# Kernel optimization log

Measured on AMD Instinct MI355X. Metric: run time of the kernel, lower is better.

## Reference

```python
import jax, jax.numpy as jnp
import numpy as np


def setup_inputs() -> dict:
    key = jax.random.key(0)
    k1, k2, k3 = jax.random.split(key, 3)
    B, S, dk = 8, 4096, 64  # per-head tensors; dk = embedding_size / h = 1024 / 16
    q = jax.random.normal(k1, (B, S, dk), dtype=jnp.float32)
    k = jax.random.normal(k2, (B, S, dk), dtype=jnp.float32)
    v = jax.random.normal(k3, (B, S, dk), dtype=jnp.float32)
    return {"q": q, "k": k, "v": v}


def reference(q, k, v):
    dk = q.shape[-1]
    # QK = q @ k^T scaled by 1/dk (NOT 1/sqrt(dk) -- faithful to source)
    scores = jnp.einsum("bqd,bkd->bqk", q, k) / dk  # [B, S, S]
    # padding mask derived from exact-zero score entries: -inf where QK == 0
    pad_mask = jnp.where(scores == 0, -jnp.inf, 0.0)
    # look-ahead (causal) mask: 0 where i >= j else -inf
    S = scores.shape[-1]
    causal = jnp.where(
        jnp.arange(S)[:, None] >= jnp.arange(S)[None, :], 0.0, -jnp.inf
    )  # [S, S]
    scores = scores + pad_mask + causal
    attn = jax.nn.softmax(scores, axis=-1)
    # NaN cleanup for fully-masked rows (softmax over all -inf)
    attn = jnp.where(jnp.isnan(attn), 0.0, attn)
    return jnp.einsum("bqk,bkd->bqd", attn, v)
```

## Files before the change

### kernel.cpp

```cpp
#include <hip/hip_runtime.h>
#include <hip/hip_bf16.h>
#include <stdint.h>

#define S_LEN 4096
#define DK    64
#define BQ    64
#define BK    64

typedef __bf16 bf16x8  __attribute__((ext_vector_type(8)));
typedef float  f32x16  __attribute__((ext_vector_type(16)));

__device__ __forceinline__ short f2bf(float f) {
    union { __bf16 h; short s; } u; u.h = (__bf16)f; return u.s;
}
__device__ __forceinline__ short4 cvt4(float4 f) {
    short4 s; s.x = f2bf(f.x); s.y = f2bf(f.y); s.z = f2bf(f.z); s.w = f2bf(f.w); return s;
}

__device__ __forceinline__ uint32_t cvtpk_bf16(float lo, float hi) {
    uint32_t d;
    asm("v_cvt_pk_bf16_f32 %0, %1, %2" : "=&v"(d) : "v"(lo), "v"(hi));
    return d;
}
__device__ __forceinline__ void plswap(uint32_t& a, uint32_t& b) {
    asm("v_permlane32_swap_b32 %0, %1" : "+v"(a), "+v"(b));
}

__device__ __forceinline__ void gload_lds16(const void* g, void* l) {
    auto gp = reinterpret_cast<const uint32_t __attribute__((address_space(1)))*>(
        reinterpret_cast<uintptr_t>(g));
    auto lp = reinterpret_cast<uint32_t __attribute__((address_space(3)))*>(
        reinterpret_cast<uintptr_t>(l));
    __builtin_amdgcn_global_load_lds(gp, lp, 16, 0, 0);
}

__device__ __forceinline__ int swz(int row) {
    return ((row ^ (row >> 3)) & 7) << 3;
}

__global__ __launch_bounds__(256) void prep_kernel(
    const float* __restrict__ K, const float* __restrict__ V,
    short* __restrict__ WK, short* __restrict__ WV)
{
    const int t = blockIdx.x, b = blockIdx.y;
    const int tid = threadIdx.x;
    const size_t ibase = ((size_t)b * S_LEN + (size_t)t * 64) * DK;
    const size_t obase = ((size_t)b * 64 + t) * 4096;
    const int r0 = tid >> 4;
    const int c0 = (tid & 15) * 4;

    #pragma unroll
    for (int i = 0; i < 4; ++i) {
        const int row = r0 + 16 * i;
        const float4 f = *reinterpret_cast<const float4*>(K + ibase + (size_t)row * DK + c0);
        *reinterpret_cast<short4*>(WK + obase + row * 64 + (c0 ^ swz(row))) = cvt4(f);
    }
    float4 vf[4];
    #pragma unroll
    for (int j = 0; j < 4; ++j)
        vf[j] = *reinterpret_cast<const float4*>(V + ibase + (size_t)(4 * r0 + j) * DK + c0);
    #pragma unroll
    for (int jj = 0; jj < 4; ++jj) {
        const int d = c0 + jj;
        short4 sp;
        sp.x = f2bf(reinterpret_cast<const float*>(&vf[0])[jj]);
        sp.y = f2bf(reinterpret_cast<const float*>(&vf[1])[jj]);
        sp.z = f2bf(reinterpret_cast<const float*>(&vf[2])[jj]);
        sp.w = f2bf(reinterpret_cast<const float*>(&vf[3])[jj]);
        *reinterpret_cast<short4*>(WV + obase + d * 64 + ((4 * r0) ^ swz(d))) = sp;
    }
}

__global__ __launch_bounds__(512, 2) void attn_kernel(
    const float* __restrict__ Q, float* __restrict__ O,
    const short* __restrict__ WK, const short* __restrict__ WV)
{
    __shared__ __align__(16) short Ks[2][16384];
    __shared__ __align__(16) short Vts[2][16384];
    __shared__ float2 Ml[4][2][32];

    const int tid  = threadIdx.x;
    const int wave = tid >> 6;
    const int lane = tid & 63;
    const int q32  = lane & 31;
    const int hi   = lane >> 5;
    const int hi4  = hi * 4;
    const int hi8  = hi * 8;
    const int grp  = wave & 3;
    const int qsub = wave >> 2;

    const int batch = blockIdx.y;
    const size_t bo = (size_t)batch * S_LEN * DK;
    const short* WKb = WK + (size_t)batch * 262144;
    const short* WVb = WV + (size_t)batch * 262144;

    auto stage_quad = [&](int quad, int buf) {
        const char* gk = (const char*)(WKb + (size_t)quad * 16384) + wave * 1024 + lane * 16;
        const char* gv = (const char*)(WVb + (size_t)quad * 16384) + wave * 1024 + lane * 16;
        char* lk = (char*)(&Ks[buf][0]) + wave * 1024;
        char* lv = (char*)(&Vts[buf][0]) + wave * 1024;
        #pragma unroll
        for (int i = 0; i < 4; ++i) {
            gload_lds16(gk + i * 8192, lk + i * 8192);
            gload_lds16(gv + i * 8192, lv + i * 8192);
        }
    };

    const float NEG_INF = -__builtin_inff();
    const float QSCALE  = 0.015625f * 1.44269504088896341f;
    const float THR     = 8.0f;
    const int swz0 = swz(q32);
    const int swz1 = swz(32 + q32);

    #pragma unroll 1
    for (int qi = 0; qi < 2; ++qi) {
        const int qb = qi ? (int)blockIdx.x : 63 - (int)blockIdx.x;
        const int q0 = qb * BQ;
        const int ntiles = qb + 1;
        const int nquads = (ntiles + 3) >> 2;
        const int qrow   = q0 + 32 * qsub + q32;

        bf16x8 qf[4];
        {
            const float* Qr = Q + bo + (size_t)qrow * DK;
            #pragma unroll
            for (int s = 0; s < 4; ++s) {
                const float4 a = *reinterpret_cast<const float4*>(Qr + 16 * s + hi8);
                const float4 b = *reinterpret_cast<const float4*>(Qr + 16 * s + hi8 + 4);
                qf[s][0] = (__bf16)(a.x * QSCALE); qf[s][1] = (__bf16)(a.y * QSCALE);
                qf[s][2] = (__bf16)(a.z * QSCALE); qf[s][3] = (__bf16)(a.w * QSCALE);
                qf[s][4] = (__bf16)(b.x * QSCALE); qf[s][5] = (__bf16)(b.y * QSCALE);
                qf[s][6] = (__bf16)(b.z * QSCALE); qf[s][7] = (__bf16)(b.w * QSCALE);
            }
        }

        float m_run = NEG_INF, l_run = 0.f;
        f32x16 oa0, oa1;
        #pragma unroll
        for (int r = 0; r < 16; ++r) { oa0[r] = 0.f; oa1[r] = 0.f; }

        stage_quad(0, 0);
        __syncthreads();

        for (int p = 0; p < nquads; ++p) {
            const int kt = 4 * p + grp;
            const bool pf = (p + 1 < nquads);
            if (pf) stage_quad(p + 1, (p + 1) & 1);

            const short* Kt = &Ks[p & 1][grp * 4096];
            const short* Vt = &Vts[p & 1][grp * 4096];
            const bool act = (kt < ntiles);

            if (act) {
                f32x16 sa0, sa1;
                #pragma unroll
                for (int r = 0; r < 16; ++r) { sa0[r] = 0.f; sa1[r] = 0.f; }
                __builtin_amdgcn_s_setprio(1);
                #pragma unroll
                for (int s = 0; s < 4; ++s) {
                    const int col = 16 * s + hi8;
                    const bf16x8 kf0 = *reinterpret_cast<const bf16x8*>(&Kt[q32 * 64 + (col ^ swz0)]);
                    const bf16x8 kf1 = *reinterpret_cast<const bf16x8*>(&Kt[(32 + q32) * 64 + (col ^ swz1)]);
                    sa0 = __builtin_amdgcn_mfma_f32_32x32x16_bf16(kf0, qf[s], sa0, 0, 0, 0);
                    sa1 = __builtin_amdgcn_mfma_f32_32x32x16_bf16(kf1, qf[s], sa1, 0, 0, 0);
                }
                __builtin_amdgcn_s_setprio(0);

                float ma[4] = {NEG_INF, NEG_INF, NEG_INF, NEG_INF};
                if (kt == qb) {
                    const int keybase = kt * BK + hi4;
                    #pragma unroll
                    for (int r = 0; r < 16; ++r) {
                        const int kl = (r & 3) + 8 * (r >> 2);
                        if (keybase + kl > qrow) sa0[r] = NEG_INF;
                        ma[r & 3] = fmaxf(ma[r & 3], sa0[r]);
                        if (keybase + kl + 32 > qrow) sa1[r] = NEG_INF;
                        ma[r & 3] = fmaxf(ma[r & 3], sa1[r]);
                    }
                } else {
                    #pragma unroll
                    for (int r = 0; r < 16; ++r) {
                        ma[r & 3] = fmaxf(ma[r & 3], sa0[r]);
                        ma[r & 3] = fmaxf(ma[r & 3], sa1[r]);
                    }
                }
                float mt = fmaxf(fmaxf(ma[0], ma[1]), fmaxf(ma[2], ma[3]));
                mt = fmaxf(mt, __shfl_xor(mt, 32));

                if (!__all(mt <= m_run + THR)) {
                    const float mnew = fmaxf(m_run, mt);
                    const float alpha = __builtin_amdgcn_exp2f(m_run - mnew);
                    m_run = mnew;
                    l_run *= alpha;
                    #pragma unroll
                    for (int r = 0; r < 16; ++r) {
                        const float ar = __shfl(alpha, (r & 3) + 8 * (r >> 2) + hi4);
                        oa0[r] *= ar; oa1[r] *= ar;
                    }
                }

                float pp[4] = {0.f, 0.f, 0.f, 0.f};
                #pragma unroll
                for (int r = 0; r < 16; ++r) {
                    sa0[r] = __builtin_amdgcn_exp2f(sa0[r] - m_run); pp[r & 3] += sa0[r];
                    sa1[r] = __builtin_amdgcn_exp2f(sa1[r] - m_run); pp[r & 3] += sa1[r];
                }
                float ps = (pp[0] + pp[1]) + (pp[2] + pp[3]);
                ps += __shfl_xor(ps, 32);
                l_run += ps;

                __builtin_amdgcn_s_setprio(1);
                #pragma unroll
                for (int c = 0; c < 2; ++c) {
                    const f32x16& sp = c ? sa1 : sa0;
                    #pragma unroll
                    for (int s2 = 0; s2 < 2; ++s2) {
                        uint32_t a0 = cvtpk_bf16(sp[8*s2+0], sp[8*s2+1]);
                        uint32_t a1 = cvtpk_bf16(sp[8*s2+2], sp[8*s2+3]);
                        uint32_t b0 = cvtpk_bf16(sp[8*s2+4], sp[8*s2+5]);
                        uint32_t b1 = cvtpk_bf16(sp[8*s2+6], sp[8*s2+7]);
                        plswap(a0, b0);
                        plswap(a1, b1);
                        union { uint32_t u[4]; bf16x8 v; } pw;
                        pw.u[0] = a0; pw.u[1] = a1; pw.u[2] = b0; pw.u[3] = b1;
                        const int vcol = 32 * c + 16 * s2 + hi8;
                        const bf16x8 vf0 = *reinterpret_cast<const bf16x8*>(&Vt[q32 * 64 + (vcol ^ swz0)]);
                        const bf16x8 vf1 = *reinterpret_cast<const bf16x8*>(&Vt[(32 + q32) * 64 + (vcol ^ swz1)]);
                        oa0 = __builtin_amdgcn_mfma_f32_32x32x16_bf16(pw.v, vf0, oa0, 0, 0, 0);
                        oa1 = __builtin_amdgcn_mfma_f32_32x32x16_bf16(pw.v, vf1, oa1, 0, 0, 0);
                    }
                }
                __builtin_amdgcn_s_setprio(0);
            }

            __syncthreads();
        }

        if (hi == 0) Ml[grp][qsub][q32] = make_float2(m_run, l_run);
        float4* Om4 = reinterpret_cast<float4*>(&Ks[0][0]);
        if (grp != 0) {
            const int midx = (grp - 1) * 2 + qsub;
            #pragma unroll
            for (int c = 0; c < 2; ++c)
                #pragma unroll
                for (int rq = 0; rq < 4; ++rq) {
                    float4 ov;
                    if (c == 0) { ov.x = oa0[4*rq]; ov.y = oa0[4*rq+1]; ov.z = oa0[4*rq+2]; ov.w = oa0[4*rq+3]; }
                    else        { ov.x = oa1[4*rq]; ov.y = oa1[4*rq+1]; ov.z = oa1[4*rq+2]; ov.w = oa1[4*rq+3]; }
                    Om4[(midx * 8 + c * 4 + rq) * 64 + lane] = ov;
                }
        }
        __syncthreads();
        if (grp == 0) {
            const float* Omf = reinterpret_cast<const float*>(&Ks[0][0]);
            float* Ob = O + bo;
            #pragma unroll
            for (int r = 0; r < 16; ++r) {
                const int row_r = (r & 3) + 8 * (r >> 2) + hi4;
                float mg[4], lg[4];
                #pragma unroll
                for (int g = 0; g < 4; ++g) {
                    const float2 v = Ml[g][qsub][row_r];
                    mg[g] = v.x; lg[g] = v.y;
                }
                const float mtot = fmaxf(fmaxf(mg[0], mg[1]), fmaxf(mg[2], mg[3]));
                float eg[4], ltot = 0.f;
                #pragma unroll
                for (int g = 0; g < 4; ++g) {
                    eg[g] = (mg[g] == NEG_INF) ? 0.f : __builtin_amdgcn_exp2f(mg[g] - mtot);
                    ltot += eg[g] * lg[g];
                }
                const float inv = (ltot > 0.f) ? (1.0f / ltot) : 0.f;
                #pragma unroll
                for (int c = 0; c < 2; ++c) {
                    float acc = eg[0] * ((c == 0) ? oa0[r] : oa1[r]);
                    #pragma unroll
                    for (int g = 1; g < 4; ++g) {
                        const int midx = (g - 1) * 2 + qsub;
                        acc += eg[g] * Omf[((midx * 8 + c * 4 + (r >> 2)) * 64 + lane) * 4 + (r & 3)];
                    }
                    Ob[(size_t)(q0 + 32 * qsub + row_r) * DK + 32 * c + q32] = acc * inv;
                }
            }
        }
        __syncthreads();
    }
}

extern "C" void kernel_launch(void* const* d_in, const int* in_sizes, int n_in,
                              void* d_out, int out_size, void* d_ws, size_t ws_size,
                              hipStream_t stream) {
    (void)in_sizes; (void)n_in; (void)out_size; (void)ws_size;
    const float* q = (const float*)d_in[0];
    const float* k = (const float*)d_in[1];
    const float* v = (const float*)d_in[2];
    float* o = (float*)d_out;
    short* wk = (short*)d_ws;
    short* wv = wk + (size_t)8 * 64 * 4096;

    hipLaunchKernelGGL(prep_kernel, dim3(64, 8), dim3(256), 0, stream, k, v, wk, wv);
    hipLaunchKernelGGL(attn_kernel, dim3(32, 8), dim3(512), 0, stream, q, o, wk, wv);
}
```

Measured before the change: 53.37 us.

## Split each key tile across two waves and use 1024-thread blocks

The block grows from 8 to 16 waves. Each key tile's 64 keys are split into two 32-key halves, each handled by its own wave with separate running max and sum, which doubles the partial softmax states. The final merge now combines 8 partials per query row through a swizzled LDS buffer, with every wave writing a float4 slice of the output. This raises parallelism and latency hiding per CU, at the cost of more reduction work, halved MFMA work per wave, and possibly lower occupancy because the launch bounds ask for 1024 threads with 4 blocks.

```diff
diff --git a/kernel.cpp b/kernel.cpp
--- a/kernel.cpp
+++ b/kernel.cpp
@@ -71,13 +71,13 @@
     }
 }
 
-__global__ __launch_bounds__(512, 2) void attn_kernel(
+__global__ __launch_bounds__(1024, 4) void attn_kernel(
     const float* __restrict__ Q, float* __restrict__ O,
     const short* __restrict__ WK, const short* __restrict__ WV)
 {
     __shared__ __align__(16) short Ks[2][16384];
     __shared__ __align__(16) short Vts[2][16384];
-    __shared__ float2 Ml[4][2][32];
+    __shared__ float2 Ml[8][2][32];
 
     const int tid  = threadIdx.x;
     const int wave = tid >> 6;
@@ -86,8 +86,10 @@
     const int hi   = lane >> 5;
     const int hi4  = hi * 4;
     const int hi8  = hi * 8;
-    const int grp  = wave & 3;
-    const int qsub = wave >> 2;
+    const int grp   = wave & 3;
+    const int khalf = (wave >> 2) & 1;
+    const int qsub  = wave >> 3;
+    const int role  = grp * 2 + khalf;
 
     const int batch = blockIdx.y;
     const size_t bo = (size_t)batch * S_LEN * DK;
@@ -95,22 +97,24 @@
     const short* WVb = WV + (size_t)batch * 262144;
 
     auto stage_quad = [&](int quad, int buf) {
-        const char* gk = (const char*)(WKb + (size_t)quad * 16384) + wave * 1024 + lane * 16;
-        const char* gv = (const char*)(WVb + (size_t)quad * 16384) + wave * 1024 + lane * 16;
-        char* lk = (char*)(&Ks[buf][0]) + wave * 1024;
-        char* lv = (char*)(&Vts[buf][0]) + wave * 1024;
+        const char* gk = (const char*)(WKb + (size_t)quad * 16384) + tid * 16;
+        const char* gv = (const char*)(WVb + (size_t)quad * 16384) + tid * 16;
+        char* lk = (char*)(&Ks[buf][0]) + tid * 16;
+        char* lv = (char*)(&Vts[buf][0]) + tid * 16;
         #pragma unroll
-        for (int i = 0; i < 4; ++i) {
-            gload_lds16(gk + i * 8192, lk + i * 8192);
-            gload_lds16(gv + i * 8192, lv + i * 8192);
+        for (int i = 0; i < 2; ++i) {
+            gload_lds16(gk + i * 16384, lk + i * 16384);
+            gload_lds16(gv + i * 16384, lv + i * 16384);
         }
     };
 
     const float NEG_INF = -__builtin_inff();
+    const float MFLOOR  = -1e38f;
     const float QSCALE  = 0.015625f * 1.44269504088896341f;
     const float THR     = 8.0f;
-    const int swz0 = swz(q32);
-    const int swz1 = swz(32 + q32);
+    const int swzK  = swz(32 * khalf + q32);
+    const int swzV0 = swz(q32);
+    const int swzV1 = swz(32 + q32);
 
     #pragma unroll 1
     for (int qi = 0; qi < 2; ++qi) {
@@ -134,7 +138,7 @@
             }
         }
 
-        float m_run = NEG_INF, l_run = 0.f;
+        float m_run = MFLOOR, l_run = 0.f;
         f32x16 oa0, oa1;
         #pragma unroll
         for (int r = 0; r < 16; ++r) { oa0[r] = 0.f; oa1[r] = 0.f; }
@@ -149,40 +153,34 @@
 
             const short* Kt = &Ks[p & 1][grp * 4096];
             const short* Vt = &Vts[p & 1][grp * 4096];
-            const bool act = (kt < ntiles);
-
-            if (act) {
-                f32x16 sa0, sa1;
-                #pragma unroll
-                for (int r = 0; r < 16; ++r) { sa0[r] = 0.f; sa1[r] = 0.f; }
+
+            if (kt < ntiles) {
+                f32x16 sa;
+                #pragma unroll
+                for (int r = 0; r < 16; ++r) sa[r] = 0.f;
                 __builtin_amdgcn_s_setprio(1);
                 #pragma unroll
                 for (int s = 0; s < 4; ++s) {
                     const int col = 16 * s + hi8;
-                    const bf16x8 kf0 = *reinterpret_cast<const bf16x8*>(&Kt[q32 * 64 + (col ^ swz0)]);
-                    const bf16x8 kf1 = *reinterpret_cast<const bf16x8*>(&Kt[(32 + q32) * 64 + (col ^ swz1)]);
-                    sa0 = __builtin_amdgcn_mfma_f32_32x32x16_bf16(kf0, qf[s], sa0, 0, 0, 0);
-                    sa1 = __builtin_amdgcn_mfma_f32_32x32x16_bf16(kf1, qf[s], sa1, 0, 0, 0);
+                    const bf16x8 kf = *reinterpret_cast<const bf16x8*>(
+                        &Kt[(32 * khalf + q32) * 64 + (col ^ swzK)]);
+                    sa = __builtin_amdgcn_mfma_f32_32x32x16_bf16(kf, qf[s], sa, 0, 0, 0);
                 }
                 __builtin_amdgcn_s_setprio(0);
 
                 float ma[4] = {NEG_INF, NEG_INF, NEG_INF, NEG_INF};
                 if (kt == qb) {
-                    const int keybase = kt * BK + hi4;
+                    const int keybase = kt * BK + 32 * khalf + hi4;
                     #pragma unroll
                     for (int r = 0; r < 16; ++r) {
                         const int kl = (r & 3) + 8 * (r >> 2);
-                        if (keybase + kl > qrow) sa0[r] = NEG_INF;
-                        ma[r & 3] = fmaxf(ma[r & 3], sa0[r]);
-                        if (keybase + kl + 32 > qrow) sa1[r] = NEG_INF;
-                        ma[r & 3] = fmaxf(ma[r & 3], sa1[r]);
+                        if (keybase + kl > qrow) sa[r] = NEG_INF;
+                        ma[r & 3] = fmaxf(ma[r & 3], sa[r]);
                     }
                 } else {
                     #pragma unroll
-                    for (int r = 0; r < 16; ++r) {
-                        ma[r & 3] = fmaxf(ma[r & 3], sa0[r]);
-                        ma[r & 3] = fmaxf(ma[r & 3], sa1[r]);
-                    }
+                    for (int r = 0; r < 16; ++r)
+                        ma[r & 3] = fmaxf(ma[r & 3], sa[r]);
                 }
                 float mt = fmaxf(fmaxf(ma[0], ma[1]), fmaxf(ma[2], ma[3]));
                 mt = fmaxf(mt, __shfl_xor(mt, 32));
@@ -202,8 +200,8 @@
                 float pp[4] = {0.f, 0.f, 0.f, 0.f};
                 #pragma unroll
                 for (int r = 0; r < 16; ++r) {
-                    sa0[r] = __builtin_amdgcn_exp2f(sa0[r] - m_run); pp[r & 3] += sa0[r];
-                    sa1[r] = __builtin_amdgcn_exp2f(sa1[r] - m_run); pp[r & 3] += sa1[r];
+                    sa[r] = __builtin_amdgcn_exp2f(sa[r] - m_run);
+                    pp[r & 3] += sa[r];
                 }
                 float ps = (pp[0] + pp[1]) + (pp[2] + pp[3]);
                 ps += __shfl_xor(ps, 32);
@@ -211,24 +209,20 @@
 
                 __builtin_amdgcn_s_setprio(1);
                 #pragma unroll
-                for (int c = 0; c < 2; ++c) {
-                    const f32x16& sp = c ? sa1 : sa0;
-                    #pragma unroll
-                    for (int s2 = 0; s2 < 2; ++s2) {
-                        uint32_t a0 = cvtpk_bf16(sp[8*s2+0], sp[8*s2+1]);
-                        uint32_t a1 = cvtpk_bf16(sp[8*s2+2], sp[8*s2+3]);
-                        uint32_t b0 = cvtpk_bf16(sp[8*s2+4], sp[8*s2+5]);
-                        uint32_t b1 = cvtpk_bf16(sp[8*s2+6], sp[8*s2+7]);
-                        plswap(a0, b0);
-                        plswap(a1, b1);
-                        union { uint32_t u[4]; bf16x8 v; } pw;
-                        pw.u[0] = a0; pw.u[1] = a1; pw.u[2] = b0; pw.u[3] = b1;
-                        const int vcol = 32 * c + 16 * s2 + hi8;
-                        const bf16x8 vf0 = *reinterpret_cast<const bf16x8*>(&Vt[q32 * 64 + (vcol ^ swz0)]);
-                        const bf16x8 vf1 = *reinterpret_cast<const bf16x8*>(&Vt[(32 + q32) * 64 + (vcol ^ swz1)]);
-                        oa0 = __builtin_amdgcn_mfma_f32_32x32x16_bf16(pw.v, vf0, oa0, 0, 0, 0);
-                        oa1 = __builtin_amdgcn_mfma_f32_32x32x16_bf16(pw.v, vf1, oa1, 0, 0, 0);
-                    }
+                for (int s2 = 0; s2 < 2; ++s2) {
+                    uint32_t a0 = cvtpk_bf16(sa[8*s2+0], sa[8*s2+1]);
+                    uint32_t a1 = cvtpk_bf16(sa[8*s2+2], sa[8*s2+3]);
+                    uint32_t b0 = cvtpk_bf16(sa[8*s2+4], sa[8*s2+5]);
+                    uint32_t b1 = cvtpk_bf16(sa[8*s2+6], sa[8*s2+7]);
+                    plswap(a0, b0);
+                    plswap(a1, b1);
+                    union { uint32_t u[4]; bf16x8 v; } pw;
+                    pw.u[0] = a0; pw.u[1] = a1; pw.u[2] = b0; pw.u[3] = b1;
+                    const int vcol = 32 * khalf + 16 * s2 + hi8;
+                    const bf16x8 vf0 = *reinterpret_cast<const bf16x8*>(&Vt[q32 * 64 + (vcol ^ swzV0)]);
+                    const bf16x8 vf1 = *reinterpret_cast<const bf16x8*>(&Vt[(32 + q32) * 64 + (vcol ^ swzV1)]);
+                    oa0 = __builtin_amdgcn_mfma_f32_32x32x16_bf16(pw.v, vf0, oa0, 0, 0, 0);
+                    oa1 = __builtin_amdgcn_mfma_f32_32x32x16_bf16(pw.v, vf1, oa1, 0, 0, 0);
                 }
                 __builtin_amdgcn_s_setprio(0);
             }
@@ -236,52 +230,53 @@
             __syncthreads();
         }
 
-        if (hi == 0) Ml[grp][qsub][q32] = make_float2(m_run, l_run);
-        float4* Om4 = reinterpret_cast<float4*>(&Ks[0][0]);
-        if (grp != 0) {
-            const int midx = (grp - 1) * 2 + qsub;
-            #pragma unroll
-            for (int c = 0; c < 2; ++c)
-                #pragma unroll
-                for (int rq = 0; rq < 4; ++rq) {
-                    float4 ov;
-                    if (c == 0) { ov.x = oa0[4*rq]; ov.y = oa0[4*rq+1]; ov.z = oa0[4*rq+2]; ov.w = oa0[4*rq+3]; }
-                    else        { ov.x = oa1[4*rq]; ov.y = oa1[4*rq+1]; ov.z = oa1[4*rq+2]; ov.w = oa1[4*rq+3]; }
-                    Om4[(midx * 8 + c * 4 + rq) * 64 + lane] = ov;
-                }
+        if (hi == 0) Ml[role][qsub][q32] = make_float2(m_run, l_run);
+        {
+            float* Obase = (qsub == 0 ? reinterpret_cast<float*>(&Ks[0][0])
+                                      : reinterpret_cast<float*>(&Vts[0][0])) + role * 2048;
+            #pragma unroll
+            for (int r = 0; r < 16; ++r) {
+                const int row = (r & 3) + 8 * (r >> 2) + hi4;
+                const int sw  = swz(row);
+                Obase[row * 64 + (q32 ^ sw)]        = oa0[r];
+                Obase[row * 64 + ((32 + q32) ^ sw)] = oa1[r];
+            }
         }
         __syncthreads();
-        if (grp == 0) {
-            const float* Omf = reinterpret_cast<const float*>(&Ks[0][0]);
-            float* Ob = O + bo;
-            #pragma unroll
-            for (int r = 0; r < 16; ++r) {
-                const int row_r = (r & 3) + 8 * (r >> 2) + hi4;
-                float mg[4], lg[4];
-                #pragma unroll
-                for (int g = 0; g < 4; ++g) {
-                    const float2 v = Ml[g][qsub][row_r];
-                    mg[g] = v.x; lg[g] = v.y;
-                }
-                const float mtot = fmaxf(fmaxf(mg[0], mg[1]), fmaxf(mg[2], mg[3]));
-                float eg[4], ltot = 0.f;
-                #pragma unroll
-                for (int g = 0; g < 4; ++g) {
-                    eg[g] = (mg[g] == NEG_INF) ? 0.f : __builtin_amdgcn_exp2f(mg[g] - mtot);
-                    ltot += eg[g] * lg[g];
-                }
-                const float inv = (ltot > 0.f) ? (1.0f / ltot) : 0.f;
-                #pragma unroll
-                for (int c = 0; c < 2; ++c) {
-                    float acc = eg[0] * ((c == 0) ? oa0[r] : oa1[r]);
-                    #pragma unroll
-                    for (int g = 1; g < 4; ++g) {
-                        const int midx = (g - 1) * 2 + qsub;
-                        acc += eg[g] * Omf[((midx * 8 + c * 4 + (r >> 2)) * 64 + lane) * 4 + (r & 3)];
-                    }
-                    Ob[(size_t)(q0 + 32 * qsub + row_r) * DK + 32 * c + q32] = acc * inv;
-                }
-            }
+        {
+            const float* Mbase = (qsub == 0 ? reinterpret_cast<const float*>(&Ks[0][0])
+                                            : reinterpret_cast<const float*>(&Vts[0][0]));
+            const int row = lane & 31;
+            const int d0  = 8 * role + 4 * hi;
+            float mg[8], lg[8];
+            #pragma unroll
+            for (int g = 0; g < 8; ++g) {
+                const float2 v = Ml[g][qsub][row];
+                mg[g] = v.x; lg[g] = v.y;
+            }
+            float mtot = MFLOOR;
+            #pragma unroll
+            for (int g = 0; g < 8; ++g) mtot = fmaxf(mtot, mg[g]);
+            float eg[8], ltot = 0.f;
+            #pragma unroll
+            for (int g = 0; g < 8; ++g) {
+                eg[g] = __builtin_amdgcn_exp2f(mg[g] - mtot);
+                ltot += eg[g] * lg[g];
+            }
+            const float inv = (ltot > 0.f) ? (1.0f / ltot) : 0.f;
+            const int sw = swz(row);
+            float acc[4] = {0.f, 0.f, 0.f, 0.f};
+            #pragma unroll
+            for (int g = 0; g < 8; ++g) {
+                const float* Pg = Mbase + g * 2048 + row * 64;
+                #pragma unroll
+                for (int j = 0; j < 4; ++j)
+                    acc[j] += eg[g] * Pg[(d0 + j) ^ sw];
+            }
+            float4 outv;
+            outv.x = acc[0] * inv; outv.y = acc[1] * inv;
+            outv.z = acc[2] * inv; outv.w = acc[3] * inv;
+            *reinterpret_cast<float4*>(O + bo + (size_t)(q0 + 32 * qsub + row) * DK + d0) = outv;
         }
         __syncthreads();
     }
@@ -299,5 +294,5 @@
     short* wv = wk + (size_t)8 * 64 * 4096;
 
     hipLaunchKernelGGL(prep_kernel, dim3(64, 8), dim3(256), 0, stream, k, v, wk, wv);
-    hipLaunchKernelGGL(attn_kernel, dim3(32, 8), dim3(512), 0, stream, q, o, wk, wv);
-}
+    hipLaunchKernelGGL(attn_kernel, dim3(32, 8), dim3(1024), 0, stream, q, o, wk, wv);
+}
```

Result: slower. 70.95 us (+32.9%).

## Defer softmax max update: exponentiate with stale max, rescale after PV

Applied to the files above, without the earlier changes.

Changes the online-softmax recurrence so that, after the first key tile, scores are exponentiated against the previous running max (clamped at exponent 60) without computing a tile max first. The P·V MFMAs are issued right away, and the max, sum and any rescale of the accumulators are applied afterwards, only when some probability exceeds 256. This takes the row-max reduction off the critical path between QK and PV and removes a serial dependency. In exchange it adds a log2 on rescale and accepts larger bf16 probability magnitudes, which risks precision loss or overflow if the clamp triggers.

```diff
diff --git a/kernel.cpp b/kernel.cpp
--- a/kernel.cpp
+++ b/kernel.cpp
@@ -107,8 +107,8 @@
     };
 
     const float NEG_INF = -__builtin_inff();
+    const float MFLOOR  = -1e38f;
     const float QSCALE  = 0.015625f * 1.44269504088896341f;
-    const float THR     = 8.0f;
     const int swz0 = swz(q32);
     const int swz1 = swz(32 + q32);
 
@@ -134,7 +134,7 @@
             }
         }
 
-        float m_run = NEG_INF, l_run = 0.f;
+        float m_run = MFLOOR, l_run = 0.f;
         f32x16 oa0, oa1;
         #pragma unroll
         for (int r = 0; r < 16; ++r) { oa0[r] = 0.f; oa1[r] = 0.f; }
@@ -149,9 +149,8 @@
 
             const short* Kt = &Ks[p & 1][grp * 4096];
             const short* Vt = &Vts[p & 1][grp * 4096];
-            const bool act = (kt < ntiles);
-
-            if (act) {
+
+            if (kt < ntiles) {
                 f32x16 sa0, sa1;
                 #pragma unroll
                 for (int r = 0; r < 16; ++r) { sa0[r] = 0.f; sa1[r] = 0.f; }
@@ -166,71 +165,115 @@
                 }
                 __builtin_amdgcn_s_setprio(0);
 
-                float ma[4] = {NEG_INF, NEG_INF, NEG_INF, NEG_INF};
                 if (kt == qb) {
                     const int keybase = kt * BK + hi4;
                     #pragma unroll
                     for (int r = 0; r < 16; ++r) {
                         const int kl = (r & 3) + 8 * (r >> 2);
                         if (keybase + kl > qrow) sa0[r] = NEG_INF;
-                        ma[r & 3] = fmaxf(ma[r & 3], sa0[r]);
                         if (keybase + kl + 32 > qrow) sa1[r] = NEG_INF;
-                        ma[r & 3] = fmaxf(ma[r & 3], sa1[r]);
-                    }
-                } else {
+                    }
+                }
+
+                if (p == 0) {
+                    float ma[4] = {NEG_INF, NEG_INF, NEG_INF, NEG_INF};
                     #pragma unroll
                     for (int r = 0; r < 16; ++r) {
                         ma[r & 3] = fmaxf(ma[r & 3], sa0[r]);
                         ma[r & 3] = fmaxf(ma[r & 3], sa1[r]);
                     }
-                }
-                float mt = fmaxf(fmaxf(ma[0], ma[1]), fmaxf(ma[2], ma[3]));
-                mt = fmaxf(mt, __shfl_xor(mt, 32));
-
-                if (!__all(mt <= m_run + THR)) {
-                    const float mnew = fmaxf(m_run, mt);
-                    const float alpha = __builtin_amdgcn_exp2f(m_run - mnew);
-                    m_run = mnew;
-                    l_run *= alpha;
-                    #pragma unroll
-                    for (int r = 0; r < 16; ++r) {
-                        const float ar = __shfl(alpha, (r & 3) + 8 * (r >> 2) + hi4);
-                        oa0[r] *= ar; oa1[r] *= ar;
-                    }
-                }
-
-                float pp[4] = {0.f, 0.f, 0.f, 0.f};
-                #pragma unroll
-                for (int r = 0; r < 16; ++r) {
-                    sa0[r] = __builtin_amdgcn_exp2f(sa0[r] - m_run); pp[r & 3] += sa0[r];
-                    sa1[r] = __builtin_amdgcn_exp2f(sa1[r] - m_run); pp[r & 3] += sa1[r];
-                }
-                float ps = (pp[0] + pp[1]) + (pp[2] + pp[3]);
-                ps += __shfl_xor(ps, 32);
-                l_run += ps;
-
-                __builtin_amdgcn_s_setprio(1);
-                #pragma unroll
-                for (int c = 0; c < 2; ++c) {
-                    const f32x16& sp = c ? sa1 : sa0;
-                    #pragma unroll
-                    for (int s2 = 0; s2 < 2; ++s2) {
-                        uint32_t a0 = cvtpk_bf16(sp[8*s2+0], sp[8*s2+1]);
-                        uint32_t a1 = cvtpk_bf16(sp[8*s2+2], sp[8*s2+3]);
-                        uint32_t b0 = cvtpk_bf16(sp[8*s2+4], sp[8*s2+5]);
-                        uint32_t b1 = cvtpk_bf16(sp[8*s2+6], sp[8*s2+7]);
-                        plswap(a0, b0);
-                        plswap(a1, b1);
-                        union { uint32_t u[4]; bf16x8 v; } pw;
-                        pw.u[0] = a0; pw.u[1] = a1; pw.u[2] = b0; pw.u[3] = b1;
-                        const int vcol = 32 * c + 16 * s2 + hi8;
-                        const bf16x8 vf0 = *reinterpret_cast<const bf16x8*>(&Vt[q32 * 64 + (vcol ^ swz0)]);
-                        const bf16x8 vf1 = *reinterpret_cast<const bf16x8*>(&Vt[(32 + q32) * 64 + (vcol ^ swz1)]);
-                        oa0 = __builtin_amdgcn_mfma_f32_32x32x16_bf16(pw.v, vf0, oa0, 0, 0, 0);
-                        oa1 = __builtin_amdgcn_mfma_f32_32x32x16_bf16(pw.v, vf1, oa1, 0, 0, 0);
-                    }
-                }
-                __builtin_amdgcn_s_setprio(0);
+                    float mt = fmaxf(fmaxf(ma[0], ma[1]), fmaxf(ma[2], ma[3]));
+                    mt = fmaxf(mt, __shfl_xor(mt, 32));
+                    m_run = fmaxf(m_run, mt);
+
+                    float pp[4] = {0.f, 0.f, 0.f, 0.f};
+                    #pragma unroll
+                    for (int r = 0; r < 16; ++r) {
+                        sa0[r] = __builtin_amdgcn_exp2f(sa0[r] - m_run); pp[r & 3] += sa0[r];
+                        sa1[r] = __builtin_amdgcn_exp2f(sa1[r] - m_run); pp[r & 3] += sa1[r];
+                    }
+                    float ps = (pp[0] + pp[1]) + (pp[2] + pp[3]);
+                    ps += __shfl_xor(ps, 32);
+                    l_run += ps;
+
+                    __builtin_amdgcn_s_setprio(1);
+                    #pragma unroll
+                    for (int c = 0; c < 2; ++c) {
+                        const f32x16& sp = c ? sa1 : sa0;
+                        #pragma unroll
+                        for (int s2 = 0; s2 < 2; ++s2) {
+                            uint32_t a0 = cvtpk_bf16(sp[8*s2+0], sp[8*s2+1]);
+                            uint32_t a1 = cvtpk_bf16(sp[8*s2+2], sp[8*s2+3]);
+                            uint32_t b0 = cvtpk_bf16(sp[8*s2+4], sp[8*s2+5]);
+                            uint32_t b1 = cvtpk_bf16(sp[8*s2+6], sp[8*s2+7]);
+                            plswap(a0, b0);
+                            plswap(a1, b1);
+                            union { uint32_t u[4]; bf16x8 v; } pw;
+                            pw.u[0] = a0; pw.u[1] = a1; pw.u[2] = b0; pw.u[3] = b1;
+                            const int vcol = 32 * c + 16 * s2 + hi8;
+                            const bf16x8 vf0 = *reinterpret_cast<const bf16x8*>(&Vt[q32 * 64 + (vcol ^ swz0)]);
+                            const bf16x8 vf1 = *reinterpret_cast<const bf16x8*>(&Vt[(32 + q32) * 64 + (vcol ^ swz1)]);
+                            oa0 = __builtin_amdgcn_mfma_f32_32x32x16_bf16(pw.v, vf0, oa0, 0, 0, 0);
+                            oa1 = __builtin_amdgcn_mfma_f32_32x32x16_bf16(pw.v, vf1, oa1, 0, 0, 0);
+                        }
+                    }
+                    __builtin_amdgcn_s_setprio(0);
+                } else {
+                    #pragma unroll
+                    for (int r = 0; r < 16; ++r) {
+                        sa0[r] = __builtin_amdgcn_exp2f(fminf(sa0[r] - m_run, 60.f));
+                        sa1[r] = __builtin_amdgcn_exp2f(fminf(sa1[r] - m_run, 60.f));
+                    }
+
+                    __builtin_amdgcn_s_setprio(1);
+                    #pragma unroll
+                    for (int c = 0; c < 2; ++c) {
+                        const f32x16& sp = c ? sa1 : sa0;
+                        #pragma unroll
+                        for (int s2 = 0; s2 < 2; ++s2) {
+                            uint32_t a0 = cvtpk_bf16(sp[8*s2+0], sp[8*s2+1]);
+                            uint32_t a1 = cvtpk_bf16(sp[8*s2+2], sp[8*s2+3]);
+                            uint32_t b0 = cvtpk_bf16(sp[8*s2+4], sp[8*s2+5]);
+                            uint32_t b1 = cvtpk_bf16(sp[8*s2+6], sp[8*s2+7]);
+                            plswap(a0, b0);
+                            plswap(a1, b1);
+                            union { uint32_t u[4]; bf16x8 v; } pw;
+                            pw.u[0] = a0; pw.u[1] = a1; pw.u[2] = b0; pw.u[3] = b1;
+                            const int vcol = 32 * c + 16 * s2 + hi8;
+                            const bf16x8 vf0 = *reinterpret_cast<const bf16x8*>(&Vt[q32 * 64 + (vcol ^ swz0)]);
+                            const bf16x8 vf1 = *reinterpret_cast<const bf16x8*>(&Vt[(32 + q32) * 64 + (vcol ^ swz1)]);
+                            oa0 = __builtin_amdgcn_mfma_f32_32x32x16_bf16(pw.v, vf0, oa0, 0, 0, 0);
+                            oa1 = __builtin_amdgcn_mfma_f32_32x32x16_bf16(pw.v, vf1, oa1, 0, 0, 0);
+                        }
+                    }
+                    __builtin_amdgcn_s_setprio(0);
+
+                    float mx[4] = {0.f, 0.f, 0.f, 0.f};
+                    float pp[4] = {0.f, 0.f, 0.f, 0.f};
+                    #pragma unroll
+                    for (int r = 0; r < 16; ++r) {
+                        mx[r & 3] = fmaxf(mx[r & 3], fmaxf(sa0[r], sa1[r]));
+                        pp[r & 3] += sa0[r] + sa1[r];
+                    }
+                    float pmax = fmaxf(fmaxf(mx[0], mx[1]), fmaxf(mx[2], mx[3]));
+                    pmax = fmaxf(pmax, __shfl_xor(pmax, 32));
+                    float ps = (pp[0] + pp[1]) + (pp[2] + pp[3]);
+                    ps += __shfl_xor(ps, 32);
+
+                    if (!__all(pmax <= 256.f)) {
+                        const float mt_rel = fmaxf(__log2f(pmax), 0.f);
+                        const float alpha  = __builtin_amdgcn_exp2f(-mt_rel);
+                        m_run += mt_rel;
+                        l_run = (l_run + ps) * alpha;
+                        #pragma unroll
+                        for (int r = 0; r < 16; ++r) {
+                            const float ar = __shfl(alpha, (r & 3) + 8 * (r >> 2) + hi4);
+                            oa0[r] *= ar; oa1[r] *= ar;
+                        }
+                    } else {
+                        l_run += ps;
+                    }
+                }
             }
 
             __syncthreads();
@@ -267,7 +310,7 @@
                 float eg[4], ltot = 0.f;
                 #pragma unroll
                 for (int g = 0; g < 4; ++g) {
-                    eg[g] = (mg[g] == NEG_INF) ? 0.f : __builtin_amdgcn_exp2f(mg[g] - mtot);
+                    eg[g] = __builtin_amdgcn_exp2f(mg[g] - mtot);
                     ltot += eg[g] * lg[g];
                 }
                 const float inv = (ltot > 0.f) ? (1.0f / ltot) : 0.f;
```

Result: slower. 56.73 us (+6.3%).
